# Performance work log

Hardware: AMD Instinct MI355X
Metric: run time of the kernel (lower is better)

## Reference

```python
import jax, jax.numpy as jnp
import numpy as np

N_NODE = 100000
N_EDGE = 640000
IN_DIM = 128
ATTN_DIM = 128
OUT_DIM = 128
N_REL_ROWS = 1005  # 2*n_rel + 5 with n_rel=500


def setup_inputs() -> dict:
    key = jax.random.key(0)
    ks = jax.random.split(key, 12)
    s = 0.05  # weight scale to keep activations sane
    return {
        "hidden": jax.random.normal(ks[0], (N_NODE, IN_DIM), dtype=jnp.float32),
        "edges": jax.random.randint(ks[1], (N_EDGE, 6), 0, N_REL_ROWS, dtype=jnp.int64),
        "kg_table": jax.random.normal(ks[2], (2, IN_DIM), dtype=jnp.float32),
        "rela_embed": jax.random.normal(ks[3], (N_REL_ROWS, IN_DIM), dtype=jnp.float32),
        "Ws_attn": jax.random.normal(ks[4], (IN_DIM, ATTN_DIM), dtype=jnp.float32) * s,
        "Wr_attn": jax.random.normal(ks[5], (IN_DIM, ATTN_DIM), dtype=jnp.float32) * s,
        "Wkg_attn_w": jax.random.normal(ks[6], (2 * IN_DIM, ATTN_DIM), dtype=jnp.float32) * s,
        "Wkg_attn_b": jax.random.normal(ks[7], (ATTN_DIM,), dtype=jnp.float32) * s,
        "w_alpha_w": jax.random.normal(ks[8], (ATTN_DIM, 1), dtype=jnp.float32) * s,
        "w_alpha_b": jax.random.normal(ks[9], (1,), dtype=jnp.float32) * s,
        "W_h": jax.random.normal(ks[10], (IN_DIM, OUT_DIM), dtype=jnp.float32) * s,
        "n_node": N_NODE,
        "left_num": 500,
    }


def reference(hidden, edges, kg_table, rela_embed, Ws_attn, Wr_attn,
              Wkg_attn_w, Wkg_attn_b, w_alpha_w, w_alpha_b, W_h,
              n_node, left_num):
    head = edges[:, 1]
    rel = edges[:, 2]
    tail = edges[:, 3]
    sub = edges[:, 4]
    obj = edges[:, 5]

    hs = hidden[sub]                      # [E, in_dim] gather
    hr = rela_embed[rel]                  # [E, in_dim]
    kg_h = kg_table[(head >= left_num).astype(jnp.int32)]  # [E, in_dim]
    kg_t = kg_table[(tail >= left_num).astype(jnp.int32)]  # [E, in_dim]
    kg = jnp.concatenate([kg_h, kg_t], axis=1)             # [E, 2*in_dim]

    # attention MLP: sigmoid(w_alpha(relu(Ws hs + Wr hr + Wkg kg + b)))
    pre = hs @ Ws_attn + hr @ Wr_attn + kg @ Wkg_attn_w + Wkg_attn_b  # [E, attn_dim]
    alpha = jax.nn.sigmoid(jax.nn.relu(pre) @ w_alpha_w + w_alpha_b)  # [E, 1]

    message = alpha * (hs + hr)                                       # [E, in_dim]
    message_agg = jax.ops.segment_sum(message, obj, num_segments=n_node)  # [n_node, in_dim]
    return message_agg @ W_h  # act = identity
```

## Files before the change

kernel.cpp:

```cpp
#include <hip/hip_runtime.h>
#include <math.h>

#define DIM   128
#define KCAP  1024
#define CW    2048
#define EPG   20
#define EPB   (EPG * 16)
#define MT2   64
#define KCH2  128
#define NKC2  (CW / KCH2)
#define NGEMM ((KCAP / MT2) * NKC2)
#define NTZ   1024
#define NB_SORT 128

typedef _Float16 h2v __attribute__((ext_vector_type(2)));
struct __align__(8)  H2x2 { h2v a, b; };
struct __align__(16) H2x4 { h2v h0, h1, h2, h3; };
__device__ inline H2x2 pack4(float4 v) {
  H2x2 r;
  r.a = h2v{(_Float16)v.x, (_Float16)v.y};
  r.b = h2v{(_Float16)v.z, (_Float16)v.w};
  return r;
}

__global__ __launch_bounds__(256) void k_pre(
    const float* __restrict__ hidden, const float* __restrict__ rela,
    const float* __restrict__ kg, const float* __restrict__ Ws,
    const float* __restrict__ Wr, const float* __restrict__ Wh,
    const float* __restrict__ Wkg, const float* __restrict__ Wkg_b,
    const int* __restrict__ edges, int n_edge, int eps,
    _Float16* __restrict__ P1h, float* __restrict__ P2, _Float16* __restrict__ P2Ch,
    float* __restrict__ T, float* __restrict__ C4,
    int* __restrict__ counts, int* __restrict__ fb_count,
    int MR, int n_rel, int NR2, int nbA, int nbP2C, int nbD) {
  __shared__ float4 smem[32 * 32];
  int t = threadIdx.x;
  int rb = blockIdx.x;
  int region;
  if (rb < nbA) region = 0;
  else if ((rb -= nbA) < nbA) region = 1;
  else if ((rb -= nbA) < nbA) region = 2;
  else if ((rb -= nbA) < nbP2C) region = 3;
  else if ((rb -= nbP2C) < nbD) region = 4;
  else if ((rb -= nbD) < 1) region = 5;
  else { rb -= 1; region = 6; }

  if (region == 5) {
    if (t == 0) *fb_count = 0;
    if (t < 64) {
      int lane = t;
      float2 c0{0,0}, c1{0,0}, c2{0,0}, c3{0,0};
      const float2* W2 = (const float2*)Wkg;
#pragma unroll 2
      for (int k = 0; k < 2 * DIM; ++k) {
        float2 w = W2[k * 64 + lane];
        int kk = k & (DIM - 1);
        float v0 = kg[kk], v1 = kg[DIM + kk];
        float s01 = (k < DIM) ? v0 : v1;
        float s10 = (k < DIM) ? v1 : v0;
        c0.x += v0 * w.x;  c0.y += v0 * w.y;
        c1.x += s01 * w.x; c1.y += s01 * w.y;
        c2.x += s10 * w.x; c2.y += s10 * w.y;
        c3.x += v1 * w.x;  c3.y += v1 * w.y;
      }
      float2 b2 = ((const float2*)Wkg_b)[lane];
      c0.x += b2.x; c0.y += b2.y; c1.x += b2.x; c1.y += b2.y;
      c2.x += b2.x; c2.y += b2.y; c3.x += b2.x; c3.y += b2.y;
      ((float2*)(C4 + 0 * DIM))[lane] = c0;
      ((float2*)(C4 + 1 * DIM))[lane] = c1;
      ((float2*)(C4 + 2 * DIM))[lane] = c2;
      ((float2*)(C4 + 3 * DIM))[lane] = c3;
    }
    return;
  }
  if (region == 6) {
    int* hist = (int*)smem;
    for (int i = t; i < KCAP; i += 256) hist[i] = 0;
    __syncthreads();
    int s = rb * eps;
    int e = s + eps; if (e > n_edge) e = n_edge;
    for (int i = s + t; i < e; i += 256) {
      int rel = edges[(long long)i * 6 + 2];
      int2 so = *(const int2*)(edges + (long long)i * 6 + 4);
      if (so.x < MR && so.y < MR && rel < NR2) atomicAdd(&hist[so.y], 1);
    }
    __syncthreads();
    for (int i = t; i < KCAP; i += 256) counts[rb * KCAP + i] = hist[i];
    return;
  }

  const float* IN; const float* W; int valid; int r0 = rb * 32;
  if (region == 0)      { IN = hidden; W = Wh; valid = MR; }
  else if (region == 1) { IN = rela;   W = Wh; valid = NR2; }
  else if (region == 2) { IN = hidden; W = Ws; valid = MR; }
  else if (region == 3) { IN = rela;   W = Wr; valid = NR2; }
  else                  { IN = rela;   W = Wr; valid = n_rel; r0 = NR2 + rb * 32; }

  const float4* in4 = (const float4*)IN;
  for (int i = t; i < 32 * 32; i += 256) {
    int row = i >> 5, q = i & 31;
    int gr = r0 + row;
    float4 v = make_float4(0.f, 0.f, 0.f, 0.f);
    if (gr < valid) v = in4[(size_t)gr * 32 + q];
    smem[i] = v;
  }
  __syncthreads();
  int cg = t & 31, rg = t >> 5;
  const float4* W4 = (const float4*)W;
  const float* sh = (const float*)smem;
  float4 a0{0,0,0,0}, a1{0,0,0,0}, a2{0,0,0,0}, a3{0,0,0,0};
#pragma unroll 8
  for (int k = 0; k < DIM; ++k) {
    float4 tv = W4[k * 32 + cg];
    float s0 = sh[(rg * 4 + 0) * DIM + k];
    float s1 = sh[(rg * 4 + 1) * DIM + k];
    float s2 = sh[(rg * 4 + 2) * DIM + k];
    float s3 = sh[(rg * 4 + 3) * DIM + k];
    a0.x += s0 * tv.x; a0.y += s0 * tv.y; a0.z += s0 * tv.z; a0.w += s0 * tv.w;
    a1.x += s1 * tv.x; a1.y += s1 * tv.y; a1.z += s1 * tv.z; a1.w += s1 * tv.w;
    a2.x += s2 * tv.x; a2.y += s2 * tv.y; a2.z += s2 * tv.z; a2.w += s2 * tv.w;
    a3.x += s3 * tv.x; a3.y += s3 * tv.y; a3.z += s3 * tv.z; a3.w += s3 * tv.w;
  }
  float4 accs[4] = {a0, a1, a2, a3};
  if (region <= 1) {
    float4* O4 = (float4*)(region == 0 ? T : T + (size_t)KCAP * DIM);
#pragma unroll
    for (int j = 0; j < 4; ++j) O4[(size_t)(r0 + rg * 4 + j) * 32 + cg] = accs[j];
    return;
  }
  if (region == 2) {
    H2x2* O = (H2x2*)P1h;
#pragma unroll
    for (int j = 0; j < 4; ++j) O[(size_t)(r0 + rg * 4 + j) * 32 + cg] = pack4(accs[j]);
    return;
  }
  if (region == 4) {
    float4* P24 = (float4*)P2;
#pragma unroll
    for (int j = 0; j < 4; ++j) P24[(size_t)(r0 + rg * 4 + j) * 32 + cg] = accs[j];
    return;
  }
  float4 S0{0,0,0,0}, S1{0,0,0,0}, S0p{0,0,0,0}, S1p{0,0,0,0};
  const float4* Wk4 = (const float4*)Wkg;
#pragma unroll 8
  for (int k = 0; k < DIM; ++k) {
    float kg0 = kg[k], kg1 = kg[DIM + k];
    float4 w0 = Wk4[k * 32 + cg];
    float4 w1 = Wk4[(DIM + k) * 32 + cg];
    S0.x += kg0 * w0.x; S0.y += kg0 * w0.y; S0.z += kg0 * w0.z; S0.w += kg0 * w0.w;
    S1.x += kg1 * w0.x; S1.y += kg1 * w0.y; S1.z += kg1 * w0.z; S1.w += kg1 * w0.w;
    S0p.x += kg0 * w1.x; S0p.y += kg0 * w1.y; S0p.z += kg0 * w1.z; S0p.w += kg0 * w1.w;
    S1p.x += kg1 * w1.x; S1p.y += kg1 * w1.y; S1p.z += kg1 * w1.z; S1p.w += kg1 * w1.w;
  }
  float4 b4 = ((const float4*)Wkg_b)[cg];
  float4 c4v[4];
  c4v[0] = make_float4(b4.x + S0.x + S0p.x, b4.y + S0.y + S0p.y, b4.z + S0.z + S0p.z, b4.w + S0.w + S0p.w);
  c4v[1] = make_float4(b4.x + S0.x + S1p.x, b4.y + S0.y + S1p.y, b4.z + S0.z + S1p.z, b4.w + S0.w + S1p.w);
  c4v[2] = make_float4(b4.x + S1.x + S0p.x, b4.y + S1.y + S0p.y, b4.z + S1.z + S0p.z, b4.w + S1.w + S0p.w);
  c4v[3] = make_float4(b4.x + S1.x + S1p.x, b4.y + S1.y + S1p.y, b4.z + S1.z + S1p.z, b4.w + S1.w + S1p.w);
  float4* P24 = (float4*)P2;
  H2x2* PC = (H2x2*)P2Ch;
#pragma unroll
  for (int j = 0; j < 4; ++j) {
    int row = r0 + rg * 4 + j;
    float4 a = accs[j];
    P24[(size_t)row * 32 + cg] = a;
#pragma unroll
    for (int c = 0; c < 4; ++c) {
      float4 v = make_float4(a.x + c4v[c].x, a.y + c4v[c].y, a.z + c4v[c].z, a.w + c4v[c].w);
      PC[((size_t)row * 4 + c) * 32 + cg] = pack4(v);
    }
  }
}

__global__ __launch_bounds__(256, 4) void k_alpha(
    const int* __restrict__ edges, int n_edge,
    const _Float16* __restrict__ P1h, const _Float16* __restrict__ P2Ch,
    const float* __restrict__ w_alpha, const float* __restrict__ w_alpha_b,
    const int* __restrict__ left_ptr, uint2* __restrict__ pa,
    int* __restrict__ fb_list, int* __restrict__ fb_count, int mr, int nr2) {
  __shared__ int seH[EPB];
  __shared__ int4 seQ[EPB];
  int base = blockIdx.x * EPB;
  int cnt = n_edge - base; if (cnt > EPB) cnt = EPB;
  if (cnt <= 0) return;
  for (int i = threadIdx.x; i < cnt; i += 256) {
    const int* ep = edges + (long long)(base + i) * 6;
    int2 ph  = *(const int2*)ep;
    int2 prt = *(const int2*)(ep + 2);
    int2 pso = *(const int2*)(ep + 4);
    seH[i] = ph.y;
    seQ[i] = make_int4(prt.x, prt.y, pso.x, pso.y);
  }
  __syncthreads();
  int g = threadIdx.x >> 4;
  int l = threadIdx.x & 15;
  int left = left_ptr[0];
  float wb = w_alpha_b[0];
  float4 wf0 = ((const float4*)w_alpha)[l * 2];
  float4 wf1 = ((const float4*)w_alpha)[l * 2 + 1];
  h2v wah0 = h2v{(_Float16)wf0.x, (_Float16)wf0.y};
  h2v wah1 = h2v{(_Float16)wf0.z, (_Float16)wf0.w};
  h2v wah2 = h2v{(_Float16)wf1.x, (_Float16)wf1.y};
  h2v wah3 = h2v{(_Float16)wf1.z, (_Float16)wf1.w};
  const h2v z2 = h2v{(_Float16)0.f, (_Float16)0.f};

  int i0 = g * EPG;
  int iend = i0 + EPG; if (iend > cnt) iend = cnt;
  if (i0 >= iend) return;

  int subA, relA, objA; bool okA; H2x4 paA, pbA;
  int subB, relB, objB; bool okB; H2x4 paB, pbB;

#define LOADI(i, rel_, sub_, obj_, ok_, pa_, pb_)                                \
  {                                                                              \
    int hh = seH[(i)];                                                           \
    int4 q = seQ[(i)];                                                           \
    rel_ = q.x; sub_ = q.z; obj_ = q.w;                                          \
    ok_ = (sub_ < mr) && (obj_ < mr) && (rel_ < nr2);                            \
    int c = ((hh >= left) ? 2 : 0) | ((q.y >= left) ? 1 : 0);                    \
    if (ok_) {                                                                   \
      pa_ = ((const H2x4*)(P1h + (size_t)sub_ * DIM))[l];                        \
      pb_ = ((const H2x4*)(P2Ch + ((size_t)(rel_ * 4 + c)) * DIM))[l];           \
    } else if (l == 0) {                                                         \
      int pos = atomicAdd(fb_count, 1);                                          \
      fb_list[pos] = base + (i);                                                 \
      pa[base + (i)] = make_uint2(0xFFFFFFFFu, 0u);                              \
    }                                                                            \
  }

#define COMP(i, rel_, sub_, obj_, ok_, pa_, pb_)                                 \
  if (ok_) {                                                                     \
    h2v acc = __builtin_elementwise_max(pa_.h0 + pb_.h0, z2) * wah0;             \
    acc += __builtin_elementwise_max(pa_.h1 + pb_.h1, z2) * wah1;                \
    acc += __builtin_elementwise_max(pa_.h2 + pb_.h2, z2) * wah2;                \
    acc += __builtin_elementwise_max(pa_.h3 + pb_.h3, z2) * wah3;                \
    float s = (float)acc[0] + (float)acc[1];                                     \
    s += __shfl_xor(s, 1); s += __shfl_xor(s, 2);                                \
    s += __shfl_xor(s, 4); s += __shfl_xor(s, 8);                                \
    if (l == 0) {                                                                \
      float av = 1.f / (1.f + expf(-(s + wb)));                                  \
      unsigned pk = (unsigned)sub_ | ((unsigned)rel_ << 10) | ((unsigned)obj_ << 20); \
      pa[base + (i)] = make_uint2(pk, __float_as_uint(av));                      \
    }                                                                            \
  }

  int icur = i0;
  LOADI(icur, relA, subA, objA, okA, paA, pbA);
  for (;;) {
    int inext = icur + 1;
    bool hasNext = inext < iend;
    if (hasNext) LOADI(inext, relB, subB, objB, okB, paB, pbB);
    COMP(icur, relA, subA, objA, okA, paA, pbA);
    if (!hasNext) break;
    icur = inext;
    int inn = icur + 1;
    bool h2 = inn < iend;
    if (h2) LOADI(inn, relA, subA, objA, okA, paA, pbA);
    COMP(icur, relB, subB, objB, okB, paB, pbB);
    if (!h2) break;
    icur = inn;
  }
#undef LOADI
#undef COMP
}

__global__ __launch_bounds__(256) void k_scatter(const uint2* __restrict__ pa, int n_edge,
                                                 int eps, const int* __restrict__ counts,
                                                 uint2* __restrict__ sorted,
                                                 int* __restrict__ off) {
  __shared__ int curs[KCAP];
  __shared__ int tot[KCAP];
  __shared__ int wsum[256];
  int b = blockIdx.x;
  int t = threadIdx.x;
  {
    int o0 = t * 4;
    int tt0 = 0, tt1 = 0, tt2 = 0, tt3 = 0;
    int pb0 = 0, pb1 = 0, pb2 = 0, pb3 = 0;
    for (int bb = 0; bb < NB_SORT; ++bb) {
      const int* row = counts + bb * KCAP + o0;
      int c0 = row[0], c1 = row[1], c2 = row[2], c3 = row[3];
      tt0 += c0; tt1 += c1; tt2 += c2; tt3 += c3;
      if (bb < b) { pb0 += c0; pb1 += c1; pb2 += c2; pb3 += c3; }
    }
    tot[o0] = tt0; tot[o0 + 1] = tt1; tot[o0 + 2] = tt2; tot[o0 + 3] = tt3;
    curs[o0] = pb0; curs[o0 + 1] = pb1; curs[o0 + 2] = pb2; curs[o0 + 3] = pb3;
  }
  __syncthreads();
  int o0 = t * 4;
  int s0 = tot[o0], s1 = tot[o0 + 1], s2 = tot[o0 + 2], s3 = tot[o0 + 3];
  wsum[t] = s0 + s1 + s2 + s3;
  __syncthreads();
  for (int d = 1; d < 256; d <<= 1) {
    int x = (t >= d) ? wsum[t - d] : 0;
    __syncthreads();
    wsum[t] += x;
    __syncthreads();
  }
  int run = (t > 0) ? wsum[t - 1] : 0;
  curs[o0]     += run;
  curs[o0 + 1] += run + s0;
  curs[o0 + 2] += run + s0 + s1;
  curs[o0 + 3] += run + s0 + s1 + s2;
  if (b == 0) {
    off[o0] = run;
    off[o0 + 1] = run + s0;
    off[o0 + 2] = run + s0 + s1;
    off[o0 + 3] = run + s0 + s1 + s2;
    if (t == 255) off[KCAP] = wsum[255];
  }
  __syncthreads();
  int s = b * eps;
  int e = s + eps; if (e > n_edge) e = n_edge;
  for (int i = s + t; i < e; i += 256) {
    uint2 v = pa[i];
    if (v.x == 0xFFFFFFFFu) continue;
    int o = (v.x >> 20) & (KCAP - 1);
    int slot = atomicAdd(&curs[o], 1);
    sorted[slot] = v;
  }
}

__global__ __launch_bounds__(256) void k_agg(const uint2* __restrict__ sorted,
                                             const int* __restrict__ off,
                                             float* __restrict__ AB) {
  __shared__ float coef[CW];
  int o = blockIdx.x;
  for (int i = threadIdx.x; i < CW; i += 256) coef[i] = 0.f;
  __syncthreads();
  int s = off[o], e = off[o + 1];
  for (int i = s + threadIdx.x; i < e; i += 256) {
    uint2 v = sorted[i];
    float a = __uint_as_float(v.y);
    atomicAdd(&coef[v.x & (KCAP - 1)], a);
    atomicAdd(&coef[KCAP + ((v.x >> 10) & (KCAP - 1))], a);
  }
  __syncthreads();
  float4* abr = (float4*)(AB + (size_t)o * CW);
  for (int i = threadIdx.x; i < CW / 4; i += 256) abr[i] = ((const float4*)coef)[i];
}

__global__ __launch_bounds__(512) void k_gemm2(const float* __restrict__ AB,
                                               const float* __restrict__ T,
                                               float* __restrict__ part,
                                               float* __restrict__ out,
                                               int n_node, int MR) {
  if (blockIdx.x >= NGEMM) {
    long long s = (long long)MR * 32;
    long long tot = (long long)n_node * 32;
    long long i = s + (long long)(blockIdx.x - NGEMM) * 512 + threadIdx.x;
    long long stride = (long long)NTZ * 512;
    float4 z{0.f, 0.f, 0.f, 0.f};
    float4* o4 = (float4*)out;
    for (; i < tot; i += stride) o4[i] = z;
    return;
  }
  __shared__ float sh[MT2][KCH2 + 4];
  int mt = blockIdx.x / NKC2;
  int kc = blockIdx.x % NKC2;
  int m0 = mt * MT2, k0 = kc * KCH2;
  for (int i = threadIdx.x; i < MT2 * (KCH2 / 4); i += 512) {
    int r = i >> 5, kq = i & 31;
    *(float4*)&sh[r][kq * 4] = *(const float4*)(AB + (long long)(m0 + r) * CW + k0 + kq * 4);
  }
  __syncthreads();
  int cg = threadIdx.x & 31;
  int rg = threadIdx.x >> 5;
  const float4* T4 = (const float4*)T;
  float4 acc0 = {0,0,0,0}, acc1 = {0,0,0,0}, acc2 = {0,0,0,0}, acc3 = {0,0,0,0};
#pragma unroll 4
  for (int k = 0; k < KCH2; ++k) {
    float4 tv = T4[(long long)(k0 + k) * (DIM / 4) + cg];
    float a0 = sh[rg * 4 + 0][k];
    float a1 = sh[rg * 4 + 1][k];
    float a2 = sh[rg * 4 + 2][k];
    float a3 = sh[rg * 4 + 3][k];
    acc0.x += a0 * tv.x; acc0.y += a0 * tv.y; acc0.z += a0 * tv.z; acc0.w += a0 * tv.w;
    acc1.x += a1 * tv.x; acc1.y += a1 * tv.y; acc1.z += a1 * tv.z; acc1.w += a1 * tv.w;
    acc2.x += a2 * tv.x; acc2.y += a2 * tv.y; acc2.z += a2 * tv.z; acc2.w += a2 * tv.w;
    acc3.x += a3 * tv.x; acc3.y += a3 * tv.y; acc3.z += a3 * tv.z; acc3.w += a3 * tv.w;
  }
  float4* p = (float4*)(part + ((long long)kc * KCAP + m0 + rg * 4) * DIM) + cg;
  p[0 * (DIM / 4)] = acc0;
  p[1 * (DIM / 4)] = acc1;
  p[2 * (DIM / 4)] = acc2;
  p[3 * (DIM / 4)] = acc3;
}

__global__ void k_outfin(const float* __restrict__ part, float* __restrict__ out, int MR) {
  long long total = (long long)MR * 32;
  long long i = (long long)blockIdx.x * blockDim.x + threadIdx.x;
  long long stride = (long long)gridDim.x * blockDim.x;
  const float4* p4 = (const float4*)part;
  float4* o4 = (float4*)out;
  for (; i < total; i += stride) {
    long long r = i >> 5;
    int c4 = (int)(i & 31);
    float4 v = {0.f, 0.f, 0.f, 0.f};
#pragma unroll
    for (int kc = 0; kc < NKC2; ++kc) {
      float4 t = p4[((long long)kc * KCAP + r) * 32 + c4];
      v.x += t.x; v.y += t.y; v.z += t.z; v.w += t.w;
    }
    o4[i] = v;
  }
}

__global__ void k_fallback(const int* __restrict__ edges, const float* __restrict__ hidden,
                           const float* __restrict__ rela, const float* __restrict__ P2,
                           const float* __restrict__ C4, const float* __restrict__ Ws,
                           const float* __restrict__ w_alpha, const float* __restrict__ w_alpha_b,
                           const float* __restrict__ Wh, const int* __restrict__ left_ptr,
                           const int* __restrict__ fb_list, const int* __restrict__ fb_count,
                           float* __restrict__ out) {
  int nfb = fb_count[0];
  if (nfb == 0) return;
  int wave = (blockIdx.x * blockDim.x + threadIdx.x) >> 6;
  int nw = (gridDim.x * blockDim.x) >> 6;
  int lane = threadIdx.x & 63;
  int left = left_ptr[0];
  for (int i = wave; i < nfb; i += nw) {
    int e = fb_list[i];
    int head = edges[(long long)e * 6 + 1];
    int rel  = edges[(long long)e * 6 + 2];
    int tail = edges[(long long)e * 6 + 3];
    int sub  = edges[(long long)e * 6 + 4];
    int obj  = edges[(long long)e * 6 + 5];
    int c = ((head >= left) ? 2 : 0) | ((tail >= left) ? 1 : 0);
    float pre0 = P2[(long long)rel * DIM + lane] + C4[c * DIM + lane];
    float pre1 = P2[(long long)rel * DIM + 64 + lane] + C4[c * DIM + 64 + lane];
    for (int k = 0; k < DIM; ++k) {
      float h = hidden[(long long)sub * DIM + k];
      pre0 += h * Ws[k * DIM + lane];
      pre1 += h * Ws[k * DIM + 64 + lane];
    }
    float s = fmaxf(pre0, 0.f) * w_alpha[lane] + fmaxf(pre1, 0.f) * w_alpha[64 + lane];
    for (int d = 1; d < 64; d <<= 1) s += __shfl_xor(s, d);
    float alpha = 1.f / (1.f + expf(-(s + w_alpha_b[0])));
    float o0 = 0.f, o1 = 0.f;
    for (int k = 0; k < DIM; ++k) {
      float m = hidden[(long long)sub * DIM + k] + rela[(long long)rel * DIM + k];
      o0 += m * Wh[k * DIM + lane];
      o1 += m * Wh[k * DIM + 64 + lane];
    }
    atomicAdd(&out[(long long)obj * DIM + lane], alpha * o0);
    atomicAdd(&out[(long long)obj * DIM + 64 + lane], alpha * o1);
  }
}

extern "C" void kernel_launch(void* const* d_in, const int* in_sizes, int n_in,
                              void* d_out, int out_size, void* d_ws, size_t ws_size,
                              hipStream_t stream) {
  const float* hidden    = (const float*)d_in[0];
  const int*   edges     = (const int*)d_in[1];
  const float* kg_table  = (const float*)d_in[2];
  const float* rela      = (const float*)d_in[3];
  const float* Ws        = (const float*)d_in[4];
  const float* Wr        = (const float*)d_in[5];
  const float* Wkg_w     = (const float*)d_in[6];
  const float* Wkg_b     = (const float*)d_in[7];
  const float* w_alpha   = (const float*)d_in[8];
  const float* w_alpha_b = (const float*)d_in[9];
  const float* Wh        = (const float*)d_in[10];
  const int*   left_ptr  = (const int*)d_in[12];

  int n_node = out_size / DIM;
  int n_edge = in_sizes[1] / 6;
  int n_rel  = in_sizes[3] / DIM;
  int MR  = n_node < KCAP ? n_node : KCAP;
  int NR2 = n_rel < KCAP ? n_rel : KCAP;
  int eps = (n_edge + NB_SORT - 1) / NB_SORT;

  int nbA   = KCAP / 32;
  int nbP2C = (NR2 + 31) / 32;
  int nbD   = (n_rel > NR2) ? (n_rel - NR2 + 31) / 32 : 0;
  int n_relpad = ((n_rel + 31) / 32) * 32;
  int NR2pad   = nbP2C * 32;

  char* ws = (char*)d_ws;
  size_t o = 0;
  auto alloc = [&](size_t b) { size_t r = o; o += (b + 255) & ~(size_t)255; return r; };
  float*    AB     = (float*)(ws + alloc((size_t)KCAP * CW * 4));
  float*    T      = (float*)(ws + alloc((size_t)CW * DIM * 4));
  _Float16* P1h    = (_Float16*)(ws + alloc((size_t)KCAP * DIM * 2));
  float*    P2     = (float*)(ws + alloc((size_t)n_relpad * DIM * 4));
  _Float16* P2Ch   = (_Float16*)(ws + alloc((size_t)NR2pad * 4 * DIM * 2));
  float*    C4     = (float*)(ws + alloc(4 * DIM * 4));
  float*    part   = (float*)(ws + alloc((size_t)NKC2 * KCAP * DIM * 4));
  uint2*    pa     = (uint2*)(ws + alloc((size_t)n_edge * 8));
  uint2*    sorted = (uint2*)(ws + alloc((size_t)n_edge * 8));
  int*      counts = (int*)(ws + alloc((size_t)NB_SORT * KCAP * 4));
  int*      off    = (int*)(ws + alloc((size_t)(KCAP + 1) * 4));
  int*      fb_list  = (int*)(ws + alloc((size_t)n_edge * 4));
  int*      fb_count = (int*)(ws + alloc(4));
  float*    out  = (float*)d_out;

  int nblocks = 3 * nbA + nbP2C + nbD + 1 + NB_SORT;
  k_pre<<<nblocks, 256, 0, stream>>>(
      hidden, rela, kg_table, Ws, Wr, Wh, Wkg_w, Wkg_b, edges, n_edge, eps,
      P1h, P2, P2Ch, T, C4, counts, fb_count, MR, n_rel, NR2, nbA, nbP2C, nbD);

  int nb = (n_edge + EPB - 1) / EPB;
  k_alpha<<<nb, 256, 0, stream>>>(edges, n_edge, P1h, P2Ch, w_alpha, w_alpha_b,
                                  left_ptr, pa, fb_list, fb_count, MR, NR2);

  k_scatter<<<NB_SORT, 256, 0, stream>>>(pa, n_edge, eps, counts, sorted, off);

  k_agg<<<KCAP, 256, 0, stream>>>(sorted, off, AB);

  k_gemm2<<<NGEMM + NTZ, 512, 0, stream>>>(AB, T, part, out, n_node, MR);
  k_outfin<<<256, 256, 0, stream>>>(part, out, MR);

  k_fallback<<<64, 256, 0, stream>>>(edges, hidden, rela, P2, C4, Ws, w_alpha,
                                     w_alpha_b, Wh, left_ptr, fb_list, fb_count, out);
}
```

Before: 119.0 us.

## Fuse counting-sort scatter into alpha kernel using per-block histogram prefix

The histogram blocks now match the alpha kernel's edge partition, one per EPB edges. A new k_prefix kernel computes per-block cursor bases and per-bucket totals from a transposed counts array. The alpha kernel then writes each edge's packed record straight into its sorted slot, so the intermediate pa array and the separate k_scatter pass go away. The costs are many more histogram blocks (about 2000 instead of 128), a cursBase buffer sized NB×KCAP that each alpha block must read, an extra kernel launch, and a block-wide prefix scan added to every alpha block.

```diff
diff --git a/kernel.cpp b/kernel.cpp
--- a/kernel.cpp
+++ b/kernel.cpp
@@ -11,7 +11,6 @@
 #define NKC2  (CW / KCH2)
 #define NGEMM ((KCAP / MT2) * NKC2)
 #define NTZ   1024
-#define NB_SORT 128
 
 typedef _Float16 h2v __attribute__((ext_vector_type(2)));
 struct __align__(8)  H2x2 { h2v a, b; };
@@ -28,11 +27,11 @@
     const float* __restrict__ kg, const float* __restrict__ Ws,
     const float* __restrict__ Wr, const float* __restrict__ Wh,
     const float* __restrict__ Wkg, const float* __restrict__ Wkg_b,
-    const int* __restrict__ edges, int n_edge, int eps,
+    const int* __restrict__ edges, int n_edge,
     _Float16* __restrict__ P1h, float* __restrict__ P2, _Float16* __restrict__ P2Ch,
     float* __restrict__ T, float* __restrict__ C4,
-    int* __restrict__ counts, int* __restrict__ fb_count,
-    int MR, int n_rel, int NR2, int nbA, int nbP2C, int nbD) {
+    int* __restrict__ counts_t, int* __restrict__ fb_count,
+    int MR, int n_rel, int NR2, int nbA, int nbP2C, int nbD, int NB) {
   __shared__ float4 smem[32 * 32];
   int t = threadIdx.x;
   int rb = blockIdx.x;
@@ -77,15 +76,15 @@
     int* hist = (int*)smem;
     for (int i = t; i < KCAP; i += 256) hist[i] = 0;
     __syncthreads();
-    int s = rb * eps;
-    int e = s + eps; if (e > n_edge) e = n_edge;
+    int s = rb * EPB;
+    int e = s + EPB; if (e > n_edge) e = n_edge;
     for (int i = s + t; i < e; i += 256) {
       int rel = edges[(long long)i * 6 + 2];
       int2 so = *(const int2*)(edges + (long long)i * 6 + 4);
       if (so.x < MR && so.y < MR && rel < NR2) atomicAdd(&hist[so.y], 1);
     }
     __syncthreads();
-    for (int i = t; i < KCAP; i += 256) counts[rb * KCAP + i] = hist[i];
+    for (int i = t; i < KCAP; i += 256) counts_t[(size_t)i * NB + rb] = hist[i];
     return;
   }
 
@@ -173,18 +172,51 @@
   }
 }
 
+__global__ __launch_bounds__(256) void k_prefix(const int* __restrict__ counts_t,
+                                                int* __restrict__ cursBase,
+                                                int* __restrict__ tot, int NB) {
+  int wv = (blockIdx.x * blockDim.x + threadIdx.x) >> 6;
+  int lane = threadIdx.x & 63;
+  if (wv >= KCAP) return;
+  const int* col = counts_t + (size_t)wv * NB;
+  int per = (NB + 63) >> 6;
+  int s = lane * per;
+  int e = s + per; if (e > NB) e = NB;
+  int sum = 0;
+  for (int i = s; i < e; ++i) sum += col[i];
+  int run = sum;
+#pragma unroll
+  for (int d = 1; d < 64; d <<= 1) {
+    int x = __shfl_up(run, d);
+    if (lane >= d) run += x;
+  }
+  int acc = run - sum;
+  if (lane == 63) tot[wv] = run;
+  for (int i = s; i < e; ++i) {
+    cursBase[(size_t)i * KCAP + wv] = acc;
+    acc += col[i];
+  }
+}
+
 __global__ __launch_bounds__(256, 4) void k_alpha(
     const int* __restrict__ edges, int n_edge,
     const _Float16* __restrict__ P1h, const _Float16* __restrict__ P2Ch,
     const float* __restrict__ w_alpha, const float* __restrict__ w_alpha_b,
-    const int* __restrict__ left_ptr, uint2* __restrict__ pa,
-    int* __restrict__ fb_list, int* __restrict__ fb_count, int mr, int nr2) {
+    const int* __restrict__ left_ptr, const int* __restrict__ tot,
+    const int* __restrict__ cursBase, int* __restrict__ off,
+    uint2* __restrict__ sorted, int* __restrict__ fb_list,
+    int* __restrict__ fb_count, int mr, int nr2) {
   __shared__ int seH[EPB];
   __shared__ int4 seQ[EPB];
-  int base = blockIdx.x * EPB;
+  __shared__ int curs[KCAP];
+  __shared__ int tots[KCAP];
+  __shared__ int wsum[256];
+  int b = blockIdx.x;
+  int t = threadIdx.x;
+  int base = b * EPB;
   int cnt = n_edge - base; if (cnt > EPB) cnt = EPB;
   if (cnt <= 0) return;
-  for (int i = threadIdx.x; i < cnt; i += 256) {
+  for (int i = t; i < cnt; i += 256) {
     const int* ep = edges + (long long)(base + i) * 6;
     int2 ph  = *(const int2*)ep;
     int2 prt = *(const int2*)(ep + 2);
@@ -192,9 +224,35 @@
     seH[i] = ph.y;
     seQ[i] = make_int4(prt.x, prt.y, pso.x, pso.y);
   }
-  __syncthreads();
-  int g = threadIdx.x >> 4;
-  int l = threadIdx.x & 15;
+  for (int i = t; i < KCAP; i += 256) tots[i] = tot[i];
+  __syncthreads();
+  int o0 = t * 4;
+  int s0 = tots[o0], s1 = tots[o0 + 1], s2 = tots[o0 + 2], s3 = tots[o0 + 3];
+  wsum[t] = s0 + s1 + s2 + s3;
+  __syncthreads();
+  for (int d = 1; d < 256; d <<= 1) {
+    int x = (t >= d) ? wsum[t - d] : 0;
+    __syncthreads();
+    wsum[t] += x;
+    __syncthreads();
+  }
+  int run = (t > 0) ? wsum[t - 1] : 0;
+  int4 cb = *(const int4*)&cursBase[(size_t)b * KCAP + o0];
+  curs[o0]     = run + cb.x;
+  curs[o0 + 1] = run + s0 + cb.y;
+  curs[o0 + 2] = run + s0 + s1 + cb.z;
+  curs[o0 + 3] = run + s0 + s1 + s2 + cb.w;
+  if (b == 0) {
+    off[o0] = run;
+    off[o0 + 1] = run + s0;
+    off[o0 + 2] = run + s0 + s1;
+    off[o0 + 3] = run + s0 + s1 + s2;
+    if (t == 255) off[KCAP] = wsum[255];
+  }
+  __syncthreads();
+
+  int g = t >> 4;
+  int l = t & 15;
   int left = left_ptr[0];
   float wb = w_alpha_b[0];
   float4 wf0 = ((const float4*)w_alpha)[l * 2];
@@ -225,7 +283,6 @@
     } else if (l == 0) {                                                         \
       int pos = atomicAdd(fb_count, 1);                                          \
       fb_list[pos] = base + (i);                                                 \
-      pa[base + (i)] = make_uint2(0xFFFFFFFFu, 0u);                              \
     }                                                                            \
   }
 
@@ -241,7 +298,8 @@
     if (l == 0) {                                                                \
       float av = 1.f / (1.f + expf(-(s + wb)));                                  \
       unsigned pk = (unsigned)sub_ | ((unsigned)rel_ << 10) | ((unsigned)obj_ << 20); \
-      pa[base + (i)] = make_uint2(pk, __float_as_uint(av));                      \
+      int slot = atomicAdd(&curs[obj_], 1);                                      \
+      sorted[slot] = make_uint2(pk, __float_as_uint(av));                        \
     }                                                                            \
   }
 
@@ -263,63 +321,6 @@
   }
 #undef LOADI
 #undef COMP
-}
-
-__global__ __launch_bounds__(256) void k_scatter(const uint2* __restrict__ pa, int n_edge,
-                                                 int eps, const int* __restrict__ counts,
-                                                 uint2* __restrict__ sorted,
-                                                 int* __restrict__ off) {
-  __shared__ int curs[KCAP];
-  __shared__ int tot[KCAP];
-  __shared__ int wsum[256];
-  int b = blockIdx.x;
-  int t = threadIdx.x;
-  {
-    int o0 = t * 4;
-    int tt0 = 0, tt1 = 0, tt2 = 0, tt3 = 0;
-    int pb0 = 0, pb1 = 0, pb2 = 0, pb3 = 0;
-    for (int bb = 0; bb < NB_SORT; ++bb) {
-      const int* row = counts + bb * KCAP + o0;
-      int c0 = row[0], c1 = row[1], c2 = row[2], c3 = row[3];
-      tt0 += c0; tt1 += c1; tt2 += c2; tt3 += c3;
-      if (bb < b) { pb0 += c0; pb1 += c1; pb2 += c2; pb3 += c3; }
-    }
-    tot[o0] = tt0; tot[o0 + 1] = tt1; tot[o0 + 2] = tt2; tot[o0 + 3] = tt3;
-    curs[o0] = pb0; curs[o0 + 1] = pb1; curs[o0 + 2] = pb2; curs[o0 + 3] = pb3;
-  }
-  __syncthreads();
-  int o0 = t * 4;
-  int s0 = tot[o0], s1 = tot[o0 + 1], s2 = tot[o0 + 2], s3 = tot[o0 + 3];
-  wsum[t] = s0 + s1 + s2 + s3;
-  __syncthreads();
-  for (int d = 1; d < 256; d <<= 1) {
-    int x = (t >= d) ? wsum[t - d] : 0;
-    __syncthreads();
-    wsum[t] += x;
-    __syncthreads();
-  }
-  int run = (t > 0) ? wsum[t - 1] : 0;
-  curs[o0]     += run;
-  curs[o0 + 1] += run + s0;
-  curs[o0 + 2] += run + s0 + s1;
-  curs[o0 + 3] += run + s0 + s1 + s2;
-  if (b == 0) {
-    off[o0] = run;
-    off[o0 + 1] = run + s0;
-    off[o0 + 2] = run + s0 + s1;
-    off[o0 + 3] = run + s0 + s1 + s2;
-    if (t == 255) off[KCAP] = wsum[255];
-  }
-  __syncthreads();
-  int s = b * eps;
-  int e = s + eps; if (e > n_edge) e = n_edge;
-  for (int i = s + t; i < e; i += 256) {
-    uint2 v = pa[i];
-    if (v.x == 0xFFFFFFFFu) continue;
-    int o = (v.x >> 20) & (KCAP - 1);
-    int slot = atomicAdd(&curs[o], 1);
-    sorted[slot] = v;
-  }
 }
 
 __global__ __launch_bounds__(256) void k_agg(const uint2* __restrict__ sorted,
@@ -470,7 +471,7 @@
   int n_rel  = in_sizes[3] / DIM;
   int MR  = n_node < KCAP ? n_node : KCAP;
   int NR2 = n_rel < KCAP ? n_rel : KCAP;
-  int eps = (n_edge + NB_SORT - 1) / NB_SORT;
+  int NB  = (n_edge + EPB - 1) / EPB;
 
   int nbA   = KCAP / 32;
   int nbP2C = (NR2 + 31) / 32;
@@ -481,31 +482,32 @@
   char* ws = (char*)d_ws;
   size_t o = 0;
   auto alloc = [&](size_t b) { size_t r = o; o += (b + 255) & ~(size_t)255; return r; };
-  float*    AB     = (float*)(ws + alloc((size_t)KCAP * CW * 4));
-  float*    T      = (float*)(ws + alloc((size_t)CW * DIM * 4));
-  _Float16* P1h    = (_Float16*)(ws + alloc((size_t)KCAP * DIM * 2));
-  float*    P2     = (float*)(ws + alloc((size_t)n_relpad * DIM * 4));
-  _Float16* P2Ch   = (_Float16*)(ws + alloc((size_t)NR2pad * 4 * DIM * 2));
-  float*    C4     = (float*)(ws + alloc(4 * DIM * 4));
-  float*    part   = (float*)(ws + alloc((size_t)NKC2 * KCAP * DIM * 4));
-  uint2*    pa     = (uint2*)(ws + alloc((size_t)n_edge * 8));
-  uint2*    sorted = (uint2*)(ws + alloc((size_t)n_edge * 8));
-  int*      counts = (int*)(ws + alloc((size_t)NB_SORT * KCAP * 4));
-  int*      off    = (int*)(ws + alloc((size_t)(KCAP + 1) * 4));
+  float*    AB       = (float*)(ws + alloc((size_t)KCAP * CW * 4));
+  float*    T        = (float*)(ws + alloc((size_t)CW * DIM * 4));
+  _Float16* P1h      = (_Float16*)(ws + alloc((size_t)KCAP * DIM * 2));
+  float*    P2       = (float*)(ws + alloc((size_t)n_relpad * DIM * 4));
+  _Float16* P2Ch     = (_Float16*)(ws + alloc((size_t)NR2pad * 4 * DIM * 2));
+  float*    C4       = (float*)(ws + alloc(4 * DIM * 4));
+  float*    part     = (float*)(ws + alloc((size_t)NKC2 * KCAP * DIM * 4));
+  uint2*    sorted   = (uint2*)(ws + alloc((size_t)n_edge * 8));
+  int*      counts_t = (int*)(ws + alloc((size_t)KCAP * NB * 4));
+  int*      cursBase = (int*)(ws + alloc((size_t)NB * KCAP * 4));
+  int*      tot      = (int*)(ws + alloc((size_t)KCAP * 4));
+  int*      off      = (int*)(ws + alloc((size_t)(KCAP + 1) * 4));
   int*      fb_list  = (int*)(ws + alloc((size_t)n_edge * 4));
   int*      fb_count = (int*)(ws + alloc(4));
   float*    out  = (float*)d_out;
 
-  int nblocks = 3 * nbA + nbP2C + nbD + 1 + NB_SORT;
+  int nblocks = 3 * nbA + nbP2C + nbD + 1 + NB;
   k_pre<<<nblocks, 256, 0, stream>>>(
-      hidden, rela, kg_table, Ws, Wr, Wh, Wkg_w, Wkg_b, edges, n_edge, eps,
-      P1h, P2, P2Ch, T, C4, counts, fb_count, MR, n_rel, NR2, nbA, nbP2C, nbD);
-
-  int nb = (n_edge + EPB - 1) / EPB;
-  k_alpha<<<nb, 256, 0, stream>>>(edges, n_edge, P1h, P2Ch, w_alpha, w_alpha_b,
-                                  left_ptr, pa, fb_list, fb_count, MR, NR2);
-
-  k_scatter<<<NB_SORT, 256, 0, stream>>>(pa, n_edge, eps, counts, sorted, off);
+      hidden, rela, kg_table, Ws, Wr, Wh, Wkg_w, Wkg_b, edges, n_edge,
+      P1h, P2, P2Ch, T, C4, counts_t, fb_count, MR, n_rel, NR2, nbA, nbP2C, nbD, NB);
+
+  k_prefix<<<KCAP / 4, 256, 0, stream>>>(counts_t, cursBase, tot, NB);
+
+  k_alpha<<<NB, 256, 0, stream>>>(edges, n_edge, P1h, P2Ch, w_alpha, w_alpha_b,
+                                  left_ptr, tot, cursBase, off, sorted,
+                                  fb_list, fb_count, MR, NR2);
 
   k_agg<<<KCAP, 256, 0, stream>>>(sorted, off, AB);
 
```

Result: slower. 127.8 us (+7.4%).
